# Kernel tuning notes

Hardware: AMD Instinct MI355X
Metric: run time of the kernel (lower is better)

Reference implementation:

```python
import math
import jax, jax.numpy as jnp
import numpy as np

H = 16  # num_heads
B, L, D = 1, 256, 1024


def setup_inputs() -> dict:
    key = jax.random.key(0)
    ks = jax.random.split(key, 12)
    s = 1.0 / math.sqrt(D)  # keep activations O(1)
    inp = {
        "mu": jax.random.normal(ks[0], (B, L, D), jnp.float32),
        "var": jax.random.uniform(ks[1], (B, L, D), jnp.float32) + 0.1,
    }
    names = ["q_mu", "q_var", "k_mu", "k_var", "v_mu", "v_var", "o_mu", "o_var"]
    for i, n in enumerate(names):
        inp["w" + n] = jax.random.normal(ks[2 + i], (D, D), jnp.float32) * s
        inp["b" + n] = jnp.zeros((D,), jnp.float32)
    return inp


def _split_heads(x):
    b, l, d = x.shape
    return x.reshape(b, l, H, d // H).transpose(0, 2, 1, 3)  # [B,H,L,Dh]


def _combine_heads(x):
    b, h, l, dh = x.shape
    return x.transpose(0, 2, 1, 3).reshape(b, l, h * dh)


def reference(mu, var, wq_mu, bq_mu, wq_var, bq_var, wk_mu, bk_mu, wk_var, bk_var,
              wv_mu, bv_mu, wv_var, bv_var, wo_mu, bo_mu, wo_var, bo_var):
    dk = mu.shape[-1] // H
    Qm = _split_heads(mu @ wq_mu + bq_mu)
    Qv = _split_heads(jax.nn.softplus(var @ wq_var + bq_var))
    Km = _split_heads(mu @ wk_mu + bk_mu)
    Kv = _split_heads(jax.nn.softplus(var @ wk_var + bk_var))
    Vm = _split_heads(mu @ wv_mu + bv_mu)
    Vv = _split_heads(jax.nn.softplus(var @ wv_var + bv_var))

    # per-element Gaussian KL, broadcast to [B,H,Lq,Lk,Dh] (as in the original)
    diff = (Qm[:, :, :, None, :] - Km[:, :, None, :, :]) ** 2
    ratio = Qv[:, :, :, None, :] / Kv[:, :, None, :, :]
    kl = diff / (2.0 * Kv[:, :, None, :, :]) + 0.5 * (ratio - jnp.log(ratio) - 1.0)
    scores = -kl.sum(-1) * (1.0 / math.sqrt(dk))  # [B,H,Lq,Lk]
    attn = jax.nn.softmax(scores, axis=-1)

    out_mu = jnp.einsum("bhqk,bhkd->bhqd", attn, Vm)
    out_var = jnp.einsum("bhqk,bhkd->bhqd", attn ** 2, Vv)

    O_mu = _combine_heads(out_mu)
    O_var = _combine_heads(out_var)
    mu_out = O_mu @ wo_mu + bo_mu
    var_out = jax.nn.softplus(O_var @ wo_var + bo_var)
    return mu_out, var_out
```

## Files before the change

kernel.cpp:

```cpp
#include <hip/hip_runtime.h>
#include <math.h>

typedef __bf16 bf16_t;
typedef bf16_t bf16x4 __attribute__((ext_vector_type(4)));
typedef bf16_t bf16x8 __attribute__((ext_vector_type(8)));
typedef float  f32x4  __attribute__((ext_vector_type(4)));

__device__ __forceinline__ float softplus_f(float x) {
    return (x > 20.f) ? x : log1pf(expf(x));
}

__device__ __forceinline__ float fast_rcp(float x) {
#if __has_builtin(__builtin_amdgcn_rcpf)
    return __builtin_amdgcn_rcpf(x);
#else
    return 1.0f / x;
#endif
}

struct PrepArgs { const float* src[8]; const float* mu; const float* var; };

__global__ __launch_bounds__(256) void prep_kernel(PrepArgs pa, bf16_t* __restrict__ wtbase,
                                                   bf16_t* __restrict__ dmu, bf16_t* __restrict__ dvar) {
    const int t = threadIdx.x;
    if (blockIdx.z == 8) {
        const int gid = (blockIdx.y * 16 + blockIdx.x) * 256 + t;
        const float* s; bf16_t* d; int off;
        if (gid < 32768) { s = pa.mu;  d = dmu;  off = gid * 8; }
        else             { s = pa.var; d = dvar; off = (gid - 32768) * 8; }
        float4 v0 = *(const float4*)(s + off);
        float4 v1 = *(const float4*)(s + off + 4);
        bf16x8 o;
        o[0] = (bf16_t)v0.x; o[1] = (bf16_t)v0.y; o[2] = (bf16_t)v0.z; o[3] = (bf16_t)v0.w;
        o[4] = (bf16_t)v1.x; o[5] = (bf16_t)v1.y; o[6] = (bf16_t)v1.z; o[7] = (bf16_t)v1.w;
        *(bf16x8*)(d + off) = o;
        return;
    }
    const int kt = blockIdx.x, nt = blockIdx.y, wm = blockIdx.z;
    const float* __restrict__ W = pa.src[wm];
    bf16_t* __restrict__ Wt = wtbase + (size_t)wm * 1048576;
    __shared__ bf16_t Ts[64][72];
    const int r0 = t >> 4, c4 = (t & 15) * 4;
#pragma unroll
    for (int rep = 0; rep < 4; ++rep) {
        const int r = r0 + rep * 16;
        const float4 v = *(const float4*)&W[(size_t)(kt * 64 + r) * 1024 + nt * 64 + c4];
        Ts[c4 + 0][r] = (bf16_t)v.x;
        Ts[c4 + 1][r] = (bf16_t)v.y;
        Ts[c4 + 2][r] = (bf16_t)v.z;
        Ts[c4 + 3][r] = (bf16_t)v.w;
    }
    __syncthreads();
#pragma unroll
    for (int rep = 0; rep < 2; ++rep) {
        const int chunk = t + rep * 256;
        const int n = chunk >> 3, kc = (chunk & 7) * 8;
        bf16x8 v = *(const bf16x8*)&Ts[n][kc];
        *(bf16x8*)&Wt[(size_t)(nt * 64 + n) * 1024 + kt * 64 + kc] = v;
    }
}

struct GemmArgs {
    const bf16_t* A[6];
    const bf16_t* Wt[6];
    const float*  bias[6];
    float*        dst[6];
    int           splus[6];
};

__global__ __launch_bounds__(256, 2) void gemm_splitk(GemmArgs args) {
    const int z = blockIdx.z;
    const bf16_t* __restrict__ A    = args.A[z];
    const bf16_t* __restrict__ Wt   = args.Wt[z];
    const float*  __restrict__ bias = args.bias[z];
    float*        __restrict__ dst  = args.dst[z];
    const int sp = args.splus[z];

    const int n_base = blockIdx.x * 64;
    const int m_base = blockIdx.y * 64;

    __shared__ __align__(16) unsigned char smem_raw[73728];
    bf16_t* stage = (bf16_t*)smem_raw;
    float*  Cr    = (float*)smem_raw;

    const int t = threadIdx.x;
    const int lane = t & 63;
    const int w = t >> 6;
    bf16_t* As = stage + w * 9216;
    bf16_t* Bs = As + 4608;

    const int r8 = lane >> 3, kb = lane & 7;
    const int fr = lane & 15, fq = lane >> 4, fk = fq * 8;

    const bf16_t* Ab = A  + (size_t)m_base * 1024 + w * 256 + kb * 8;
    const bf16_t* Bb = Wt + (size_t)n_base * 1024 + w * 256 + kb * 8;

    f32x4 acc[4][4] = {};

    bf16x8 pa[8], pb[8];
#pragma unroll
    for (int i = 0; i < 8; ++i) {
        pa[i] = *(const bf16x8*)(Ab + (size_t)(i * 8 + r8) * 1024);
        pb[i] = *(const bf16x8*)(Bb + (size_t)(i * 8 + r8) * 1024);
    }

#pragma unroll
    for (int s = 0; s < 4; ++s) {
#pragma unroll
        for (int i = 0; i < 8; ++i) {
            *(bf16x8*)&As[(i * 8 + r8) * 72 + kb * 8] = pa[i];
            *(bf16x8*)&Bs[(i * 8 + r8) * 72 + kb * 8] = pb[i];
        }
        if (s < 3) {
            const int off = (s + 1) * 64;
#pragma unroll
            for (int i = 0; i < 8; ++i) {
                pa[i] = *(const bf16x8*)(Ab + (size_t)(i * 8 + r8) * 1024 + off);
                pb[i] = *(const bf16x8*)(Bb + (size_t)(i * 8 + r8) * 1024 + off);
            }
        }
#pragma unroll
        for (int kh = 0; kh < 2; ++kh) {
            bf16x8 aF[4], bF[4];
#pragma unroll
            for (int i = 0; i < 4; ++i)
                aF[i] = *(const bf16x8*)&As[(i * 16 + fr) * 72 + kh * 32 + fk];
#pragma unroll
            for (int j = 0; j < 4; ++j)
                bF[j] = *(const bf16x8*)&Bs[(j * 16 + fr) * 72 + kh * 32 + fk];
#pragma unroll
            for (int i = 0; i < 4; ++i)
#pragma unroll
                for (int j = 0; j < 4; ++j)
                    acc[i][j] = __builtin_amdgcn_mfma_f32_16x16x32_bf16(aF[i], bF[j], acc[i][j], 0, 0, 0);
        }
    }

    __syncthreads();
    {
        float* Crw = Cr + w * 4352;
        const int orow = fq * 4;
#pragma unroll
        for (int i = 0; i < 4; ++i)
#pragma unroll
            for (int j = 0; j < 4; ++j)
#pragma unroll
                for (int rr = 0; rr < 4; ++rr)
                    Crw[(i * 16 + orow + rr) * 68 + j * 16 + fr] = acc[i][j][rr];
    }
    __syncthreads();

    const int cc = (t & 15) * 4;
    f32x4 bv4 = *(const f32x4*)&bias[n_base + cc];
#pragma unroll
    for (int i = 0; i < 4; ++i) {
        const int row = (t >> 4) + i * 16;
        f32x4 s0 = *(const f32x4*)&Cr[0 * 4352 + row * 68 + cc];
        f32x4 s1 = *(const f32x4*)&Cr[1 * 4352 + row * 68 + cc];
        f32x4 s2 = *(const f32x4*)&Cr[2 * 4352 + row * 68 + cc];
        f32x4 s3 = *(const f32x4*)&Cr[3 * 4352 + row * 68 + cc];
        f32x4 v = (s0 + s1) + (s2 + s3) + bv4;
        if (sp) {
            v[0] = softplus_f(v[0]); v[1] = softplus_f(v[1]);
            v[2] = softplus_f(v[2]); v[3] = softplus_f(v[3]);
        }
        *(f32x4*)&dst[(size_t)(m_base + row) * 1024 + n_base + cc] = v;
    }
}

__global__ __launch_bounds__(256) void feat_kernel(const float* __restrict__ Km,
                                                   const float* __restrict__ Kv,
                                                   bf16_t* __restrict__ Gbf,
                                                   float* __restrict__ cvec) {
    const int h = blockIdx.x, kb = blockIdx.y;
    const int t = threadIdx.x;
    const int kx = t & 63;
    const int dg = t >> 6;
    const int katt = kb * 64 + kx;
    const float* kvp = Kv + (size_t)katt * 1024 + h * 64 + dg * 16;
    const float* kmp = Km + (size_t)katt * 1024 + h * 64 + dg * 16;
    bf16_t* grow = Gbf + ((size_t)(h * 256 + katt)) * 128;
    float cp = 0.f;
#pragma unroll
    for (int c = 0; c < 4; ++c) {
        f32x4 kv = *(const f32x4*)(kvp + c * 4);
        f32x4 km = *(const f32x4*)(kmp + c * 4);
        bf16x4 o1, o2;
#pragma unroll
        for (int e = 0; e < 4; ++e) {
            const float r = 0.5f * fast_rcp(kv[e]);
            o1[e] = (bf16_t)r;
            o2[e] = (bf16_t)(-2.f * km[e] * r);
            cp += km[e] * km[e] * r + 0.5f * __logf(kv[e]);
        }
        *(bf16x4*)&grow[dg * 16 + c * 4]      = o1;
        *(bf16x4*)&grow[64 + dg * 16 + c * 4] = o2;
    }
    __shared__ float red[4][64];
    red[dg][kx] = cp;
    __syncthreads();
    if (dg == 0)
        cvec[h * 256 + katt] = red[0][kx] + red[1][kx] + red[2][kx] + red[3][kx];
}

#define OFF_VM   0
#define OFF_VV   36864
#define OFF_FS   73728
#define OFF_SC   82176
#define OFF_PHI  98816
#define OFF_PLO  107264
#define OFF_P2H  115712
#define OFF_P2L  124160
#define ATTN_SMEM 132608

__global__ __launch_bounds__(512) void attn_v7(const float* __restrict__ Qm,
                                               const float* __restrict__ Qv,
                                               const bf16_t* __restrict__ Gbf,
                                               const float* __restrict__ cvec,
                                               const float* __restrict__ Vm,
                                               const float* __restrict__ Vv,
                                               bf16_t* __restrict__ Omu,
                                               bf16_t* __restrict__ Ovar) {
    __shared__ __align__(16) unsigned char smem[ATTN_SMEM];
    bf16_t* Vsm = (bf16_t*)(smem + OFF_VM);
    bf16_t* Vsv = (bf16_t*)(smem + OFF_VV);
    float*  Fs  = (float*)(smem + OFF_FS);
    float*  Sc  = (float*)(smem + OFF_SC);
    bf16_t* Phi = (bf16_t*)(smem + OFF_PHI);
    bf16_t* Plo = (bf16_t*)(smem + OFF_PLO);
    bf16_t* P2h = (bf16_t*)(smem + OFF_P2H);
    bf16_t* P2l = (bf16_t*)(smem + OFF_P2L);

    const int qt = blockIdx.x, h = blockIdx.y;
    const int t = threadIdx.x, w = t >> 6, lane = t & 63;
    const int fr = lane & 15, fq = lane >> 4;
    const int n0 = w * 32;

    const bf16_t* gB = Gbf + ((size_t)(h * 256 + n0 + fr)) * 128 + fq * 8;

    bf16x8 bcur[4];
#pragma unroll
    for (int ks = 0; ks < 4; ++ks) bcur[ks] = *(const bf16x8*)(gB + ks * 32);

    if (t < 256) {
        const int r = t >> 4, c = t & 15;
        f32x4 qm = *(const f32x4*)(Qm + (size_t)(qt * 16 + r) * 1024 + h * 64 + c * 4);
        f32x4 qv = *(const f32x4*)(Qv + (size_t)(qt * 16 + r) * 1024 + h * 64 + c * 4);
        *(f32x4*)&Fs[r * 132 + c * 4]      = qm * qm + qv;
        *(f32x4*)&Fs[r * 132 + 64 + c * 4] = qm;
    }
    __syncthreads();

    bf16x8 ahi[4], alo[4];
#pragma unroll
    for (int ks = 0; ks < 4; ++ks) {
        f32x4 f0 = *(const f32x4*)&Fs[fr * 132 + ks * 32 + fq * 8];
        f32x4 f1 = *(const f32x4*)&Fs[fr * 132 + ks * 32 + fq * 8 + 4];
#pragma unroll
        for (int e = 0; e < 4; ++e) {
            bf16_t hb = (bf16_t)f0[e];
            ahi[ks][e] = hb; alo[ks][e] = (bf16_t)(f0[e] - (float)hb);
            bf16_t hb2 = (bf16_t)f1[e];
            ahi[ks][e + 4] = hb2; alo[ks][e + 4] = (bf16_t)(f1[e] - (float)hb2);
        }
    }

    const int tm = t & 255;
// ... 94 lines not shown
        *(bf16x4*)&P2h[row * 264 + lane * 4] = p2hi;
        *(bf16x4*)&P2l[row * 264 + lane * 4] = p2lo;
    }
    __syncthreads();

    const int tile = w & 3;
    const int isvar = w >> 2;
    const bf16_t* Pa = isvar ? P2h : Phi;
    const bf16_t* Pb = isvar ? P2l : Plo;
    const bf16_t* Vs = isvar ? Vsv : Vsm;
    f32x4 accp = {0.f, 0.f, 0.f, 0.f};
#pragma unroll
    for (int k0 = 0; k0 < 256; k0 += 32) {
        const int ka = k0 + fq * 8;
        bf16x8 a1 = *(const bf16x8*)&Pa[fr * 264 + ka];
        bf16x8 a2 = *(const bf16x8*)&Pb[fr * 264 + ka];
        bf16x8 bfr;
#pragma unroll
        for (int j = 0; j < 8; ++j)
            bfr[j] = Vs[(ka + j) * 72 + tile * 16 + fr];
        accp = __builtin_amdgcn_mfma_f32_16x16x32_bf16(a1, bfr, accp, 0, 0, 0);
        accp = __builtin_amdgcn_mfma_f32_16x16x32_bf16(a2, bfr, accp, 0, 0, 0);
    }

    bf16_t* Out = isvar ? Ovar : Omu;
#pragma unroll
    for (int reg = 0; reg < 4; ++reg) {
        const int qg = qt * 16 + fq * 4 + reg;
        const size_t ob = (size_t)qg * 1024 + h * 64 + tile * 16 + fr;
        Out[ob] = (bf16_t)accp[reg];
    }
}

extern "C" void kernel_launch(void* const* d_in, const int* in_sizes, int n_in,
                              void* d_out, int out_size, void* d_ws, size_t ws_size,
                              hipStream_t stream) {
    const float* mu  = (const float*)d_in[0];
    const float* var = (const float*)d_in[1];

    uint8_t* ws = (uint8_t*)d_ws;
    bf16_t* Abf_mu  = (bf16_t*)(ws);
    bf16_t* Abf_var = (bf16_t*)(ws + (512u << 10));
    bf16_t* WtB     = (bf16_t*)(ws + (1u << 20));
    float*  Proj    = (float*)(ws + (17u << 20));
    bf16_t* Obf_mu  = (bf16_t*)(ws + (23u << 20));
    bf16_t* Obf_var = (bf16_t*)(ws + (23u << 20) + (512u << 10));
    bf16_t* Gbf     = (bf16_t*)(ws + (24u << 20));
    float*  cvec    = (float*)(ws + (25u << 20));

    PrepArgs pa;
    for (int i = 0; i < 8; ++i) pa.src[i] = (const float*)d_in[2 + 2 * i];
    pa.mu = mu; pa.var = var;
    prep_kernel<<<dim3(16, 16, 9), 256, 0, stream>>>(pa, WtB, Abf_mu, Abf_var);

    GemmArgs g1;
    for (int z = 0; z < 6; ++z) {
        g1.A[z]    = (z & 1) ? Abf_var : Abf_mu;
        g1.Wt[z]   = WtB + (size_t)z * 1048576;
        g1.bias[z] = (const float*)d_in[3 + 2 * z];
        g1.dst[z]  = Proj + (size_t)z * 262144;
        g1.splus[z] = (z & 1);
    }
    gemm_splitk<<<dim3(16, 4, 6), 256, 0, stream>>>(g1);

    feat_kernel<<<dim3(16, 4), 256, 0, stream>>>(Proj + 2 * 262144, Proj + 3 * 262144, Gbf, cvec);

    attn_v7<<<dim3(16, 16), 512, 0, stream>>>(Proj,
                                              Proj + 262144,
                                              Gbf, cvec,
                                              Proj + 4 * 262144,
                                              Proj + 5 * 262144,
                                              Obf_mu, Obf_var);

    GemmArgs g3;
    for (int z = 0; z < 6; ++z) {
        g3.A[z]    = Obf_mu;
        g3.Wt[z]   = WtB + (size_t)6 * 1048576;
        g3.bias[z] = (const float*)d_in[15];
        g3.dst[z]  = (float*)d_out;
        g3.splus[z] = 0;
    }
    g3.A[1]    = Obf_var;
    g3.Wt[1]   = WtB + (size_t)7 * 1048576;
    g3.bias[1] = (const float*)d_in[17];
    g3.dst[1]  = (float*)d_out + 262144;
    g3.splus[1] = 1;
    gemm_splitk<<<dim3(16, 4, 2), 256, 0, stream>>>(g3);
}
```

Measured before the change: 150.4 us.

## Fuse whole pipeline into one cooperative persistent kernel with grid syncs

Replaces the chain of prep, projection GEMM, feature, attention and output GEMM launches with a single cooperative kernel of 256 blocks that runs each stage in turn, separated by grid-wide barriers. The projection GEMMs now read fp32 activations and convert them in-register, which removes the activation prep pass. The K projections are fused with the KL feature computation, and the GEMM K-split is widened to 8 waves. The aim is to cut launch overhead and intermediate passes, at the cost of grid-sync latency and fixed occupancy; the old multi-kernel path is kept as a fallback if the cooperative launch fails.

```diff
diff --git a/kernel.cpp b/kernel.cpp
--- a/kernel.cpp
+++ b/kernel.cpp
@@ -1,5 +1,8 @@
 #include <hip/hip_runtime.h>
+#include <hip/hip_cooperative_groups.h>
 #include <math.h>
+
+namespace cg = cooperative_groups;
 
 typedef __bf16 bf16_t;
 typedef bf16_t bf16x4 __attribute__((ext_vector_type(4)));
@@ -16,191 +19,6 @@
 #else
     return 1.0f / x;
 #endif
-}
-
-struct PrepArgs { const float* src[8]; const float* mu; const float* var; };
-
-__global__ __launch_bounds__(256) void prep_kernel(PrepArgs pa, bf16_t* __restrict__ wtbase,
-                                                   bf16_t* __restrict__ dmu, bf16_t* __restrict__ dvar) {
-    const int t = threadIdx.x;
-    if (blockIdx.z == 8) {
-        const int gid = (blockIdx.y * 16 + blockIdx.x) * 256 + t;
-        const float* s; bf16_t* d; int off;
-        if (gid < 32768) { s = pa.mu;  d = dmu;  off = gid * 8; }
-        else             { s = pa.var; d = dvar; off = (gid - 32768) * 8; }
-        float4 v0 = *(const float4*)(s + off);
-        float4 v1 = *(const float4*)(s + off + 4);
-        bf16x8 o;
-        o[0] = (bf16_t)v0.x; o[1] = (bf16_t)v0.y; o[2] = (bf16_t)v0.z; o[3] = (bf16_t)v0.w;
-        o[4] = (bf16_t)v1.x; o[5] = (bf16_t)v1.y; o[6] = (bf16_t)v1.z; o[7] = (bf16_t)v1.w;
-        *(bf16x8*)(d + off) = o;
-        return;
-    }
-    const int kt = blockIdx.x, nt = blockIdx.y, wm = blockIdx.z;
-    const float* __restrict__ W = pa.src[wm];
-    bf16_t* __restrict__ Wt = wtbase + (size_t)wm * 1048576;
-    __shared__ bf16_t Ts[64][72];
-    const int r0 = t >> 4, c4 = (t & 15) * 4;
-#pragma unroll
-    for (int rep = 0; rep < 4; ++rep) {
-        const int r = r0 + rep * 16;
-        const float4 v = *(const float4*)&W[(size_t)(kt * 64 + r) * 1024 + nt * 64 + c4];
-        Ts[c4 + 0][r] = (bf16_t)v.x;
-        Ts[c4 + 1][r] = (bf16_t)v.y;
-        Ts[c4 + 2][r] = (bf16_t)v.z;
-        Ts[c4 + 3][r] = (bf16_t)v.w;
-    }
-    __syncthreads();
-#pragma unroll
-    for (int rep = 0; rep < 2; ++rep) {
-        const int chunk = t + rep * 256;
-        const int n = chunk >> 3, kc = (chunk & 7) * 8;
-        bf16x8 v = *(const bf16x8*)&Ts[n][kc];
-        *(bf16x8*)&Wt[(size_t)(nt * 64 + n) * 1024 + kt * 64 + kc] = v;
-    }
-}
-
-struct GemmArgs {
-    const bf16_t* A[6];
-    const bf16_t* Wt[6];
-    const float*  bias[6];
-    float*        dst[6];
-    int           splus[6];
-};
-
-__global__ __launch_bounds__(256, 2) void gemm_splitk(GemmArgs args) {
-    const int z = blockIdx.z;
-    const bf16_t* __restrict__ A    = args.A[z];
-    const bf16_t* __restrict__ Wt   = args.Wt[z];
-    const float*  __restrict__ bias = args.bias[z];
-    float*        __restrict__ dst  = args.dst[z];
-    const int sp = args.splus[z];
-
-    const int n_base = blockIdx.x * 64;
-    const int m_base = blockIdx.y * 64;
-
-    __shared__ __align__(16) unsigned char smem_raw[73728];
-    bf16_t* stage = (bf16_t*)smem_raw;
-    float*  Cr    = (float*)smem_raw;
-
-    const int t = threadIdx.x;
-    const int lane = t & 63;
-    const int w = t >> 6;
-    bf16_t* As = stage + w * 9216;
-    bf16_t* Bs = As + 4608;
-
-    const int r8 = lane >> 3, kb = lane & 7;
-    const int fr = lane & 15, fq = lane >> 4, fk = fq * 8;
-
-    const bf16_t* Ab = A  + (size_t)m_base * 1024 + w * 256 + kb * 8;
-    const bf16_t* Bb = Wt + (size_t)n_base * 1024 + w * 256 + kb * 8;
-
-    f32x4 acc[4][4] = {};
-
-    bf16x8 pa[8], pb[8];
-#pragma unroll
-    for (int i = 0; i < 8; ++i) {
-        pa[i] = *(const bf16x8*)(Ab + (size_t)(i * 8 + r8) * 1024);
-        pb[i] = *(const bf16x8*)(Bb + (size_t)(i * 8 + r8) * 1024);
-    }
-
-#pragma unroll
-    for (int s = 0; s < 4; ++s) {
-#pragma unroll
-        for (int i = 0; i < 8; ++i) {
-            *(bf16x8*)&As[(i * 8 + r8) * 72 + kb * 8] = pa[i];
-            *(bf16x8*)&Bs[(i * 8 + r8) * 72 + kb * 8] = pb[i];
-        }
-        if (s < 3) {
-            const int off = (s + 1) * 64;
-#pragma unroll
-            for (int i = 0; i < 8; ++i) {
-                pa[i] = *(const bf16x8*)(Ab + (size_t)(i * 8 + r8) * 1024 + off);
-                pb[i] = *(const bf16x8*)(Bb + (size_t)(i * 8 + r8) * 1024 + off);
-            }
-        }
-#pragma unroll
-        for (int kh = 0; kh < 2; ++kh) {
-            bf16x8 aF[4], bF[4];
-#pragma unroll
-            for (int i = 0; i < 4; ++i)
-                aF[i] = *(const bf16x8*)&As[(i * 16 + fr) * 72 + kh * 32 + fk];
-#pragma unroll
-            for (int j = 0; j < 4; ++j)
-                bF[j] = *(const bf16x8*)&Bs[(j * 16 + fr) * 72 + kh * 32 + fk];
-#pragma unroll
-            for (int i = 0; i < 4; ++i)
-#pragma unroll
-                for (int j = 0; j < 4; ++j)
-                    acc[i][j] = __builtin_amdgcn_mfma_f32_16x16x32_bf16(aF[i], bF[j], acc[i][j], 0, 0, 0);
-        }
-    }
-
-    __syncthreads();
-    {
-        float* Crw = Cr + w * 4352;
-        const int orow = fq * 4;
-#pragma unroll
-        for (int i = 0; i < 4; ++i)
-#pragma unroll
-            for (int j = 0; j < 4; ++j)
-#pragma unroll
-                for (int rr = 0; rr < 4; ++rr)
-                    Crw[(i * 16 + orow + rr) * 68 + j * 16 + fr] = acc[i][j][rr];
-    }
-    __syncthreads();
-
-    const int cc = (t & 15) * 4;
-    f32x4 bv4 = *(const f32x4*)&bias[n_base + cc];
-#pragma unroll
-    for (int i = 0; i < 4; ++i) {
-        const int row = (t >> 4) + i * 16;
-        f32x4 s0 = *(const f32x4*)&Cr[0 * 4352 + row * 68 + cc];
-        f32x4 s1 = *(const f32x4*)&Cr[1 * 4352 + row * 68 + cc];
-        f32x4 s2 = *(const f32x4*)&Cr[2 * 4352 + row * 68 + cc];
-        f32x4 s3 = *(const f32x4*)&Cr[3 * 4352 + row * 68 + cc];
-        f32x4 v = (s0 + s1) + (s2 + s3) + bv4;
-        if (sp) {
-            v[0] = softplus_f(v[0]); v[1] = softplus_f(v[1]);
-            v[2] = softplus_f(v[2]); v[3] = softplus_f(v[3]);
-        }
-        *(f32x4*)&dst[(size_t)(m_base + row) * 1024 + n_base + cc] = v;
-    }
-}
-
-__global__ __launch_bounds__(256) void feat_kernel(const float* __restrict__ Km,
-                                                   const float* __restrict__ Kv,
-                                                   bf16_t* __restrict__ Gbf,
-                                                   float* __restrict__ cvec) {
-    const int h = blockIdx.x, kb = blockIdx.y;
-    const int t = threadIdx.x;
-    const int kx = t & 63;
-    const int dg = t >> 6;
-    const int katt = kb * 64 + kx;
-    const float* kvp = Kv + (size_t)katt * 1024 + h * 64 + dg * 16;
-    const float* kmp = Km + (size_t)katt * 1024 + h * 64 + dg * 16;
-    bf16_t* grow = Gbf + ((size_t)(h * 256 + katt)) * 128;
-    float cp = 0.f;
-#pragma unroll
-    for (int c = 0; c < 4; ++c) {
-        f32x4 kv = *(const f32x4*)(kvp + c * 4);
-        f32x4 km = *(const f32x4*)(kmp + c * 4);
-        bf16x4 o1, o2;
-#pragma unroll
-        for (int e = 0; e < 4; ++e) {
-            const float r = 0.5f * fast_rcp(kv[e]);
-            o1[e] = (bf16_t)r;
-            o2[e] = (bf16_t)(-2.f * km[e] * r);
-            cp += km[e] * km[e] * r + 0.5f * __logf(kv[e]);
-        }
-        *(bf16x4*)&grow[dg * 16 + c * 4]      = o1;
-        *(bf16x4*)&grow[64 + dg * 16 + c * 4] = o2;
-    }
-    __shared__ float red[4][64];
-    red[dg][kx] = cp;
-    __syncthreads();
-    if (dg == 0)
-        cvec[h * 256 + katt] = red[0][kx] + red[1][kx] + red[2][kx] + red[3][kx];
 }
 
 #define OFF_VM   0
@@ -213,15 +31,11 @@
 #define OFF_P2L  124160
 #define ATTN_SMEM 132608
 
-__global__ __launch_bounds__(512) void attn_v7(const float* __restrict__ Qm,
-                                               const float* __restrict__ Qv,
-                                               const bf16_t* __restrict__ Gbf,
-                                               const float* __restrict__ cvec,
-                                               const float* __restrict__ Vm,
-                                               const float* __restrict__ Vv,
-                                               bf16_t* __restrict__ Omu,
-                                               bf16_t* __restrict__ Ovar) {
-    __shared__ __align__(16) unsigned char smem[ATTN_SMEM];
+__device__ void attn_body(unsigned char* smem, const int t, const int qt, const int h,
+                          const float* __restrict__ Qm, const float* __restrict__ Qv,
+                          const bf16_t* __restrict__ Gbf, const float* __restrict__ cvec,
+                          const float* __restrict__ Vm, const float* __restrict__ Vv,
+                          bf16_t* __restrict__ Omu, bf16_t* __restrict__ Ovar) {
     bf16_t* Vsm = (bf16_t*)(smem + OFF_VM);
     bf16_t* Vsv = (bf16_t*)(smem + OFF_VV);
     float*  Fs  = (float*)(smem + OFF_FS);
@@ -231,8 +45,7 @@
     bf16_t* P2h = (bf16_t*)(smem + OFF_P2H);
     bf16_t* P2l = (bf16_t*)(smem + OFF_P2L);
 
-    const int qt = blockIdx.x, h = blockIdx.y;
-    const int t = threadIdx.x, w = t >> 6, lane = t & 63;
+    const int w = t >> 6, lane = t & 63;
     const int fr = lane & 15, fq = lane >> 4;
     const int n0 = w * 32;
 
@@ -393,13 +206,493 @@
     }
 }
 
+#define FUSED_SMEM 147456
+
+struct FusedArgs {
+    const float* mu; const float* var;
+    const float* W[8];
+    const float* Bias[8];
+    bf16_t* WtB;
+    float*  Proj;
+    bf16_t* Obm; bf16_t* Obv;
+    bf16_t* Gbf; float* cvec;
+    float* out_mu; float* out_var;
+};
+
+template<bool AF32>
+__device__ __forceinline__ void gemm_core(const void* Aptr, const bf16_t* __restrict__ Wt,
+                                          const int m_base, const int n_base,
+                                          unsigned char* smem, const int t, f32x4 out[2]) {
+    __syncthreads();
+    bf16_t* stage = (bf16_t*)smem;
+    float*  Cr    = (float*)smem;
+    const int lane = t & 63, w = t >> 6;
+    bf16_t* As = stage + w * 9216;
+    bf16_t* Bs = As + 4608;
+    const int r8 = lane >> 3, kb = lane & 7;
+    const int fr = lane & 15, fq = lane >> 4, fk = fq * 8;
+
+    const bf16_t* Bb = Wt + (size_t)n_base * 1024 + w * 128 + kb * 8;
+    const float*  Af = (const float*)Aptr  + (size_t)m_base * 1024 + w * 128 + kb * 8;
+    const bf16_t* Ab = (const bf16_t*)Aptr + (size_t)m_base * 1024 + w * 128 + kb * 8;
+
+    f32x4 acc[4][4] = {};
+    bf16x8 pb[8];
+    f32x4 paf0[8], paf1[8];
+    bf16x8 pa[8];
+#pragma unroll
+    for (int i = 0; i < 8; ++i) {
+        pb[i] = *(const bf16x8*)(Bb + (size_t)(i * 8 + r8) * 1024);
+        if constexpr (AF32) {
+            paf0[i] = *(const f32x4*)(Af + (size_t)(i * 8 + r8) * 1024);
+            paf1[i] = *(const f32x4*)(Af + (size_t)(i * 8 + r8) * 1024 + 4);
+        } else {
+            pa[i] = *(const bf16x8*)(Ab + (size_t)(i * 8 + r8) * 1024);
+        }
+    }
+
+#pragma unroll
+    for (int s = 0; s < 2; ++s) {
+#pragma unroll
+        for (int i = 0; i < 8; ++i) {
+            bf16x8 av;
+            if constexpr (AF32) {
+#pragma unroll
+                for (int e = 0; e < 4; ++e) {
+                    av[e]     = (bf16_t)paf0[i][e];
+                    av[e + 4] = (bf16_t)paf1[i][e];
+                }
+            } else {
+                av = pa[i];
+            }
+            *(bf16x8*)&As[(i * 8 + r8) * 72 + kb * 8] = av;
+            *(bf16x8*)&Bs[(i * 8 + r8) * 72 + kb * 8] = pb[i];
+        }
+        if (s == 0) {
+#pragma unroll
+            for (int i = 0; i < 8; ++i) {
+                pb[i] = *(const bf16x8*)(Bb + (size_t)(i * 8 + r8) * 1024 + 64);
+                if constexpr (AF32) {
+                    paf0[i] = *(const f32x4*)(Af + (size_t)(i * 8 + r8) * 1024 + 64);
+                    paf1[i] = *(const f32x4*)(Af + (size_t)(i * 8 + r8) * 1024 + 68);
+                } else {
+                    pa[i] = *(const bf16x8*)(Ab + (size_t)(i * 8 + r8) * 1024 + 64);
+                }
+            }
+        }
+#pragma unroll
+        for (int kh = 0; kh < 2; ++kh) {
+            bf16x8 aF[4], bF[4];
+#pragma unroll
+            for (int i = 0; i < 4; ++i)
+                aF[i] = *(const bf16x8*)&As[(i * 16 + fr) * 72 + kh * 32 + fk];
+#pragma unroll
+            for (int j = 0; j < 4; ++j)
+                bF[j] = *(const bf16x8*)&Bs[(j * 16 + fr) * 72 + kh * 32 + fk];
+#pragma unroll
+            for (int i = 0; i < 4; ++i)
+#pragma unroll
+                for (int j = 0; j < 4; ++j)
+                    acc[i][j] = __builtin_amdgcn_mfma_f32_16x16x32_bf16(aF[i], bF[j], acc[i][j], 0, 0, 0);
+        }
+    }
+
+    __syncthreads();
+    {
+        float* Crw = Cr + w * 4352;
+        const int orow = fq * 4;
+#pragma unroll
+        for (int i = 0; i < 4; ++i)
+#pragma unroll
+            for (int j = 0; j < 4; ++j)
+#pragma unroll
+                for (int rr = 0; rr < 4; ++rr)
+                    Crw[(i * 16 + orow + rr) * 68 + j * 16 + fr] = acc[i][j][rr];
+    }
+    __syncthreads();
+
+    const int cc = (t & 15) * 4;
+#pragma unroll
+    for (int i = 0; i < 2; ++i) {
+        const int row = (t >> 4) + i * 32;
+        f32x4 v = {0.f, 0.f, 0.f, 0.f};
+#pragma unroll
+        for (int sl = 0; sl < 8; ++sl)
+            v += *(const f32x4*)&Cr[sl * 4352 + row * 68 + cc];
+        out[i] = v;
+    }
+}
+
+__device__ __forceinline__ void run_simple(const FusedArgs& a, unsigned char* smem,
+                                           const int t, const int st) {
+    const int z4 = st >> 6, rem = st & 63;
+    const int nb = (rem >> 2) * 64, mb = (rem & 3) * 64;
+    const int wi = (z4 < 2) ? z4 : (z4 + 2);
+    const void* A = (z4 & 1) ? (const void*)a.var : (const void*)a.mu;
+    f32x4 o[2];
+    gemm_core<true>(A, a.WtB + (size_t)wi * 1048576, mb, nb, smem, t, o);
+    const int cc = (t & 15) * 4;
+    const f32x4 bv = *(const f32x4*)&a.Bias[wi][nb + cc];
+    float* dst = a.Proj + (size_t)z4 * 262144;
+    const int sp = z4 & 1;
+#pragma unroll
+    for (int i = 0; i < 2; ++i) {
+        const int row = (t >> 4) + i * 32;
+        f32x4 v = o[i] + bv;
+        if (sp) {
+            v[0] = softplus_f(v[0]); v[1] = softplus_f(v[1]);
+            v[2] = softplus_f(v[2]); v[3] = softplus_f(v[3]);
+        }
+        *(f32x4*)&dst[(size_t)(mb + row) * 1024 + nb + cc] = v;
+    }
+}
+
+__device__ __forceinline__ void run_fusedK(const FusedArgs& a, unsigned char* smem,
+                                           const int t, const int ft) {
+    const int nb = (ft >> 2) * 64, mb = (ft & 3) * 64;
+    const int h = ft >> 2;
+    f32x4 okm[2], okv[2];
+    gemm_core<true>(a.mu,  a.WtB + (size_t)2 * 1048576, mb, nb, smem, t, okm);
+    gemm_core<true>(a.var, a.WtB + (size_t)3 * 1048576, mb, nb, smem, t, okv);
+    const int cc = (t & 15) * 4;
+    const f32x4 bkm = *(const f32x4*)&a.Bias[2][nb + cc];
+    const f32x4 bkv = *(const f32x4*)&a.Bias[3][nb + cc];
+    float cp[2];
+#pragma unroll
+    for (int i = 0; i < 2; ++i) {
+        const int row = (t >> 4) + i * 32;
+        const int katt = mb + row;
+        const f32x4 km  = okm[i] + bkm;
+        const f32x4 kvr = okv[i] + bkv;
+        bf16x4 o1, o2;
+        float c = 0.f;
+#pragma unroll
+        for (int e = 0; e < 4; ++e) {
+            const float kv = softplus_f(kvr[e]);
+            const float r  = 0.5f * fast_rcp(kv);
+            o1[e] = (bf16_t)r;
+            o2[e] = (bf16_t)(-2.f * km[e] * r);
+            c += km[e] * km[e] * r + 0.5f * __logf(kv);
+        }
+        bf16_t* grow = a.Gbf + ((size_t)(h * 256 + katt)) * 128;
+        *(bf16x4*)&grow[cc]      = o1;
+        *(bf16x4*)&grow[64 + cc] = o2;
+        cp[i] = c;
+    }
+    __syncthreads();
+    float* red = (float*)smem;
+#pragma unroll
+    for (int i = 0; i < 2; ++i)
+        red[((t >> 4) + i * 32) * 16 + (t & 15)] = cp[i];
+    __syncthreads();
+    if (t < 64) {
+        float s = 0.f;
+#pragma unroll
+        for (int g = 0; g < 16; ++g) s += red[t * 16 + g];
+        a.cvec[h * 256 + mb + t] = s;
+    }
+}
+
+__global__ __launch_bounds__(512) void fused_all(FusedArgs a) {
+    __shared__ __align__(16) unsigned char smem[FUSED_SMEM];
+    cg::grid_group grid = cg::this_grid();
+    const int blk = blockIdx.x;
+    const int t = threadIdx.x;
+
+    {
+        bf16_t* Ts = (bf16_t*)smem + (t >> 8) * 4608;
+        const int lt = t & 255;
+        const int r0 = lt >> 4, c4 = (lt & 15) * 4;
+        for (int it = 0; it < 4; ++it) {
+            const int tt = blk * 8 + it * 2 + (t >> 8);
+            const int wm = tt >> 8, rem = tt & 255, kt = rem >> 4, nt = rem & 15;
+            const float* __restrict__ W = a.W[wm];
+            bf16_t* __restrict__ Wt = a.WtB + (size_t)wm * 1048576;
+#pragma unroll
+            for (int rep = 0; rep < 4; ++rep) {
+                const int r = r0 + rep * 16;
+                const float4 v = *(const float4*)&W[(size_t)(kt * 64 + r) * 1024 + nt * 64 + c4];
+                Ts[(c4 + 0) * 72 + r] = (bf16_t)v.x;
+                Ts[(c4 + 1) * 72 + r] = (bf16_t)v.y;
+                Ts[(c4 + 2) * 72 + r] = (bf16_t)v.z;
+                Ts[(c4 + 3) * 72 + r] = (bf16_t)v.w;
+            }
+            __syncthreads();
+#pragma unroll
+            for (int rep = 0; rep < 2; ++rep) {
+                const int chunk = lt + rep * 256;
+                const int n = chunk >> 3, kc = (chunk & 7) * 8;
+                bf16x8 v = *(const bf16x8*)&Ts[n * 72 + kc];
+                *(bf16x8*)&Wt[(size_t)(nt * 64 + n) * 1024 + kt * 64 + kc] = v;
+            }
+            __syncthreads();
+        }
+    }
+    __threadfence();
+    grid.sync();
+
+    if (blk < 192) {
+        run_simple(a, smem, t, blk);
+        if (blk < 64) run_simple(a, smem, t, 192 + blk);
+    } else {
+        run_fusedK(a, smem, t, blk - 192);
+    }
+    __threadfence();
+    grid.sync();
+
+    attn_body(smem, t, blk >> 4, blk & 15,
+              a.Proj, a.Proj + 262144, a.Gbf, a.cvec,
+              a.Proj + 2 * 262144, a.Proj + 3 * 262144, a.Obm, a.Obv);
+    __threadfence();
+    grid.sync();
+
+    if (blk < 128) {
+        const int z = blk >> 6, rem = blk & 63;
+        const int nb = (rem >> 2) * 64, mb = (rem & 3) * 64;
+        f32x4 o[2];
+        gemm_core<false>(z ? (const void*)a.Obv : (const void*)a.Obm,
+                         a.WtB + (size_t)(6 + z) * 1048576, mb, nb, smem, t, o);
+        const int cc = (t & 15) * 4;
+        const f32x4 bv = *(const f32x4*)&a.Bias[6 + z][nb + cc];
+        float* dst = z ? a.out_var : a.out_mu;
+#pragma unroll
+        for (int i = 0; i < 2; ++i) {
+            const int row = (t >> 4) + i * 32;
+            f32x4 v = o[i] + bv;
+            if (z) {
+                v[0] = softplus_f(v[0]); v[1] = softplus_f(v[1]);
+                v[2] = softplus_f(v[2]); v[3] = softplus_f(v[3]);
+            }
+            *(f32x4*)&dst[(size_t)(mb + row) * 1024 + nb + cc] = v;
+        }
+    }
+}
+
+struct PrepArgs { const float* src[8]; const float* mu; const float* var; };
+
+__global__ __launch_bounds__(256) void prep_kernel(PrepArgs pa, bf16_t* __restrict__ wtbase,
+                                                   bf16_t* __restrict__ dmu, bf16_t* __restrict__ dvar) {
+    const int t = threadIdx.x;
+    if (blockIdx.z == 8) {
+        const int gid = (blockIdx.y * 16 + blockIdx.x) * 256 + t;
+        const float* s; bf16_t* d; int off;
+        if (gid < 32768) { s = pa.mu;  d = dmu;  off = gid * 8; }
+        else             { s = pa.var; d = dvar; off = (gid - 32768) * 8; }
+        float4 v0 = *(const float4*)(s + off);
+        float4 v1 = *(const float4*)(s + off + 4);
+        bf16x8 o;
+        o[0] = (bf16_t)v0.x; o[1] = (bf16_t)v0.y; o[2] = (bf16_t)v0.z; o[3] = (bf16_t)v0.w;
+        o[4] = (bf16_t)v1.x; o[5] = (bf16_t)v1.y; o[6] = (bf16_t)v1.z; o[7] = (bf16_t)v1.w;
+        *(bf16x8*)(d + off) = o;
+        return;
+    }
+    const int kt = blockIdx.x, nt = blockIdx.y, wm = blockIdx.z;
+    const float* __restrict__ W = pa.src[wm];
+    bf16_t* __restrict__ Wt = wtbase + (size_t)wm * 1048576;
+    __shared__ bf16_t Ts[64][72];
+    const int r0 = t >> 4, c4 = (t & 15) * 4;
+#pragma unroll
+    for (int rep = 0; rep < 4; ++rep) {
+        const int r = r0 + rep * 16;
+        const float4 v = *(const float4*)&W[(size_t)(kt * 64 + r) * 1024 + nt * 64 + c4];
+        Ts[c4 + 0][r] = (bf16_t)v.x;
+        Ts[c4 + 1][r] = (bf16_t)v.y;
+        Ts[c4 + 2][r] = (bf16_t)v.z;
+        Ts[c4 + 3][r] = (bf16_t)v.w;
+    }
+    __syncthreads();
+#pragma unroll
+    for (int rep = 0; rep < 2; ++rep) {
+        const int chunk = t + rep * 256;
+        const int n = chunk >> 3, kc = (chunk & 7) * 8;
+        bf16x8 v = *(const bf16x8*)&Ts[n][kc];
+        *(bf16x8*)&Wt[(size_t)(nt * 64 + n) * 1024 + kt * 64 + kc] = v;
+    }
+}
+
+struct GemmArgs {
+    const bf16_t* A[6];
+    const bf16_t* Wt[6];
+    const float*  bias[6];
+    float*        dst[6];
+    int           splus[6];
+};
+
+__global__ __launch_bounds__(256, 2) void gemm_splitk(GemmArgs args) {
+    const int z = blockIdx.z;
+    const bf16_t* __restrict__ A    = args.A[z];
+    const bf16_t* __restrict__ Wt   = args.Wt[z];
+    const float*  __restrict__ bias = args.bias[z];
+    float*        __restrict__ dst  = args.dst[z];
+    const int sp = args.splus[z];
+
+    const int n_base = blockIdx.x * 64;
+    const int m_base = blockIdx.y * 64;
+
+    __shared__ __align__(16) unsigned char smem_raw[73728];
+    bf16_t* stage = (bf16_t*)smem_raw;
+    float*  Cr    = (float*)smem_raw;
+
+    const int t = threadIdx.x;
+    const int lane = t & 63;
+    const int w = t >> 6;
+    bf16_t* As = stage + w * 9216;
+    bf16_t* Bs = As + 4608;
+
+    const int r8 = lane >> 3, kb = lane & 7;
+    const int fr = lane & 15, fq = lane >> 4, fk = fq * 8;
+
+    const bf16_t* Ab = A  + (size_t)m_base * 1024 + w * 256 + kb * 8;
+    const bf16_t* Bb = Wt + (size_t)n_base * 1024 + w * 256 + kb * 8;
+
+    f32x4 acc[4][4] = {};
+
+    bf16x8 pa[8], pb[8];
+#pragma unroll
+    for (int i = 0; i < 8; ++i) {
+        pa[i] = *(const bf16x8*)(Ab + (size_t)(i * 8 + r8) * 1024);
+        pb[i] = *(const bf16x8*)(Bb + (size_t)(i * 8 + r8) * 1024);
+    }
+
+#pragma unroll
+    for (int s = 0; s < 4; ++s) {
+#pragma unroll
+        for (int i = 0; i < 8; ++i) {
+            *(bf16x8*)&As[(i * 8 + r8) * 72 + kb * 8] = pa[i];
+            *(bf16x8*)&Bs[(i * 8 + r8) * 72 + kb * 8] = pb[i];
+        }
+        if (s < 3) {
+            const int off = (s + 1) * 64;
+#pragma unroll
+            for (int i = 0; i < 8; ++i) {
+                pa[i] = *(const bf16x8*)(Ab + (size_t)(i * 8 + r8) * 1024 + off);
+                pb[i] = *(const bf16x8*)(Bb + (size_t)(i * 8 + r8) * 1024 + off);
+            }
+        }
+#pragma unroll
+        for (int kh = 0; kh < 2; ++kh) {
+            bf16x8 aF[4], bF[4];
+#pragma unroll
+            for (int i = 0; i < 4; ++i)
+                aF[i] = *(const bf16x8*)&As[(i * 16 + fr) * 72 + kh * 32 + fk];
+#pragma unroll
+            for (int j = 0; j < 4; ++j)
+                bF[j] = *(const bf16x8*)&Bs[(j * 16 + fr) * 72 + kh * 32 + fk];
+#pragma unroll
+            for (int i = 0; i < 4; ++i)
+#pragma unroll
+                for (int j = 0; j < 4; ++j)
+                    acc[i][j] = __builtin_amdgcn_mfma_f32_16x16x32_bf16(aF[i], bF[j], acc[i][j], 0, 0, 0);
+        }
+    }
+
+    __syncthreads();
+    {
+        float* Crw = Cr + w * 4352;
+        const int orow = fq * 4;
+#pragma unroll
+        for (int i = 0; i < 4; ++i)
+#pragma unroll
+            for (int j = 0; j < 4; ++j)
+#pragma unroll
+                for (int rr = 0; rr < 4; ++rr)
+                    Crw[(i * 16 + orow + rr) * 68 + j * 16 + fr] = acc[i][j][rr];
+    }
+    __syncthreads();
+
+    const int cc = (t & 15) * 4;
+    f32x4 bv4 = *(const f32x4*)&bias[n_base + cc];
+#pragma unroll
+    for (int i = 0; i < 4; ++i) {
+        const int row = (t >> 4) + i * 16;
+        f32x4 s0 = *(const f32x4*)&Cr[0 * 4352 + row * 68 + cc];
+        f32x4 s1 = *(const f32x4*)&Cr[1 * 4352 + row * 68 + cc];
+        f32x4 s2 = *(const f32x4*)&Cr[2 * 4352 + row * 68 + cc];
+        f32x4 s3 = *(const f32x4*)&Cr[3 * 4352 + row * 68 + cc];
+        f32x4 v = (s0 + s1) + (s2 + s3) + bv4;
+        if (sp) {
+            v[0] = softplus_f(v[0]); v[1] = softplus_f(v[1]);
+            v[2] = softplus_f(v[2]); v[3] = softplus_f(v[3]);
+        }
+        *(f32x4*)&dst[(size_t)(m_base + row) * 1024 + n_base + cc] = v;
+    }
+}
+
+__global__ __launch_bounds__(256) void feat_kernel(const float* __restrict__ Km,
+                                                   const float* __restrict__ Kv,
+                                                   bf16_t* __restrict__ Gbf,
+                                                   float* __restrict__ cvec) {
+    const int h = blockIdx.x, kb = blockIdx.y;
+    const int t = threadIdx.x;
+    const int kx = t & 63;
+    const int dg = t >> 6;
+    const int katt = kb * 64 + kx;
+    const float* kvp = Kv + (size_t)katt * 1024 + h * 64 + dg * 16;
+    const float* kmp = Km + (size_t)katt * 1024 + h * 64 + dg * 16;
+    bf16_t* grow = Gbf + ((size_t)(h * 256 + katt)) * 128;
+    float cp = 0.f;
+#pragma unroll
+    for (int c = 0; c < 4; ++c) {
+        f32x4 kv = *(const f32x4*)(kvp + c * 4);
+        f32x4 km = *(const f32x4*)(kmp + c * 4);
+        bf16x4 o1, o2;
+#pragma unroll
+        for (int e = 0; e < 4; ++e) {
+            const float r = 0.5f * fast_rcp(kv[e]);
+            o1[e] = (bf16_t)r;
+            o2[e] = (bf16_t)(-2.f * km[e] * r);
+            cp += km[e] * km[e] * r + 0.5f * __logf(kv[e]);
+        }
+        *(bf16x4*)&grow[dg * 16 + c * 4]      = o1;
+        *(bf16x4*)&grow[64 + dg * 16 + c * 4] = o2;
+    }
+    __shared__ float red[4][64];
+    red[dg][kx] = cp;
+    __syncthreads();
+    if (dg == 0)
+        cvec[h * 256 + katt] = red[0][kx] + red[1][kx] + red[2][kx] + red[3][kx];
+}
+
+__global__ __launch_bounds__(512) void attn_v7(const float* __restrict__ Qm,
+                                               const float* __restrict__ Qv,
+                                               const bf16_t* __restrict__ Gbf,
+                                               const float* __restrict__ cvec,
+                                               const float* __restrict__ Vm,
+                                               const float* __restrict__ Vv,
+                                               bf16_t* __restrict__ Omu,
+                                               bf16_t* __restrict__ Ovar) {
+    __shared__ __align__(16) unsigned char smem[ATTN_SMEM];
+    attn_body(smem, threadIdx.x, blockIdx.x, blockIdx.y, Qm, Qv, Gbf, cvec, Vm, Vv, Omu, Ovar);
+}
+
 extern "C" void kernel_launch(void* const* d_in, const int* in_sizes, int n_in,
                               void* d_out, int out_size, void* d_ws, size_t ws_size,
                               hipStream_t stream) {
     const float* mu  = (const float*)d_in[0];
     const float* var = (const float*)d_in[1];
-
     uint8_t* ws = (uint8_t*)d_ws;
+
+    FusedArgs fa;
+    fa.mu = mu; fa.var = var;
+    for (int i = 0; i < 8; ++i) {
+        fa.W[i]    = (const float*)d_in[2 + 2 * i];
+        fa.Bias[i] = (const float*)d_in[3 + 2 * i];
+    }
+    fa.WtB  = (bf16_t*)(ws);
+    fa.Proj = (float*)(ws + (16u << 20));
+    fa.Obm  = (bf16_t*)(ws + (20u << 20));
+    fa.Obv  = (bf16_t*)(ws + (20u << 20) + (512u << 10));
+    fa.Gbf  = (bf16_t*)(ws + (21u << 20));
+    fa.cvec = (float*)(ws + (22u << 20));
+    fa.out_mu  = (float*)d_out;
+    fa.out_var = (float*)d_out + 262144;
+
+    void* kp[] = { &fa };
+    hipError_t err = hipLaunchCooperativeKernel((void*)fused_all, dim3(256), dim3(512),
+                                                kp, 0, stream);
+    if (err == hipSuccess) return;
+    (void)hipGetLastError();
+
     bf16_t* Abf_mu  = (bf16_t*)(ws);
     bf16_t* Abf_var = (bf16_t*)(ws + (512u << 10));
     bf16_t* WtB     = (bf16_t*)(ws + (1u << 20));
@@ -426,11 +719,8 @@
 
     feat_kernel<<<dim3(16, 4), 256, 0, stream>>>(Proj + 2 * 262144, Proj + 3 * 262144, Gbf, cvec);
 
-    attn_v7<<<dim3(16, 16), 512, 0, stream>>>(Proj,
-                                              Proj + 262144,
-                                              Gbf, cvec,
-                                              Proj + 4 * 262144,
-                                              Proj + 5 * 262144,
+    attn_v7<<<dim3(16, 16), 512, 0, stream>>>(Proj, Proj + 262144, Gbf, cvec,
+                                              Proj + 4 * 262144, Proj + 5 * 262144,
                                               Obf_mu, Obf_var);
 
     GemmArgs g3;
```

New measurement: 396.1 us. +163.4%, slower.

## Fuse input bf16 cast into projection GEMM and K-feature prep into K-projection

Applied to the files above, without the earlier changes.

The projection GEMM now reads the fp32 mu/var directly and converts them to bf16 while staging into LDS, so the separate cast pass in the prep kernel is gone. The K-mean and K-variance projections are computed together in one block, which then writes the Gbf features and the cvec constants directly, removing feat_kernel and the fp32 Km/Kv round-trip through global memory. This saves one launch and some traffic, but the fused K blocks do two GEMMs each, creating a slower tail within a grid of 320 blocks. The fp32 A loads also double the A-side load bytes and register use.

```diff
diff --git a/kernel.cpp b/kernel.cpp
--- a/kernel.cpp
+++ b/kernel.cpp
@@ -18,24 +18,10 @@
 #endif
 }
 
-struct PrepArgs { const float* src[8]; const float* mu; const float* var; };
-
-__global__ __launch_bounds__(256) void prep_kernel(PrepArgs pa, bf16_t* __restrict__ wtbase,
-                                                   bf16_t* __restrict__ dmu, bf16_t* __restrict__ dvar) {
+struct PrepArgs { const float* src[8]; };
+
+__global__ __launch_bounds__(256) void prep_kernel(PrepArgs pa, bf16_t* __restrict__ wtbase) {
     const int t = threadIdx.x;
-    if (blockIdx.z == 8) {
-        const int gid = (blockIdx.y * 16 + blockIdx.x) * 256 + t;
-        const float* s; bf16_t* d; int off;
-        if (gid < 32768) { s = pa.mu;  d = dmu;  off = gid * 8; }
-        else             { s = pa.var; d = dvar; off = (gid - 32768) * 8; }
-        float4 v0 = *(const float4*)(s + off);
-        float4 v1 = *(const float4*)(s + off + 4);
-        bf16x8 o;
-        o[0] = (bf16_t)v0.x; o[1] = (bf16_t)v0.y; o[2] = (bf16_t)v0.z; o[3] = (bf16_t)v0.w;
-        o[4] = (bf16_t)v1.x; o[5] = (bf16_t)v1.y; o[6] = (bf16_t)v1.z; o[7] = (bf16_t)v1.w;
-        *(bf16x8*)(d + off) = o;
-        return;
-    }
     const int kt = blockIdx.x, nt = blockIdx.y, wm = blockIdx.z;
     const float* __restrict__ W = pa.src[wm];
     bf16_t* __restrict__ Wt = wtbase + (size_t)wm * 1048576;
@@ -60,63 +46,65 @@
     }
 }
 
-struct GemmArgs {
-    const bf16_t* A[6];
-    const bf16_t* Wt[6];
-    const float*  bias[6];
-    float*        dst[6];
-    int           splus[6];
-};
-
-__global__ __launch_bounds__(256, 2) void gemm_splitk(GemmArgs args) {
-    const int z = blockIdx.z;
-    const bf16_t* __restrict__ A    = args.A[z];
-    const bf16_t* __restrict__ Wt   = args.Wt[z];
-    const float*  __restrict__ bias = args.bias[z];
-    float*        __restrict__ dst  = args.dst[z];
-    const int sp = args.splus[z];
-
-    const int n_base = blockIdx.x * 64;
-    const int m_base = blockIdx.y * 64;
-
-    __shared__ __align__(16) unsigned char smem_raw[73728];
-    bf16_t* stage = (bf16_t*)smem_raw;
-    float*  Cr    = (float*)smem_raw;
-
-    const int t = threadIdx.x;
-    const int lane = t & 63;
-    const int w = t >> 6;
+template<bool AF32>
+__device__ __forceinline__ void gemm4_core(const void* Aptr, const bf16_t* __restrict__ Wt,
+                                           const int m_base, const int n_base,
+                                           unsigned char* smem, const int t, f32x4 out[4]) {
+    __syncthreads();
+    bf16_t* stage = (bf16_t*)smem;
+    float*  Cr    = (float*)smem;
+    const int lane = t & 63, w = t >> 6;
     bf16_t* As = stage + w * 9216;
     bf16_t* Bs = As + 4608;
-
     const int r8 = lane >> 3, kb = lane & 7;
     const int fr = lane & 15, fq = lane >> 4, fk = fq * 8;
 
-    const bf16_t* Ab = A  + (size_t)m_base * 1024 + w * 256 + kb * 8;
     const bf16_t* Bb = Wt + (size_t)n_base * 1024 + w * 256 + kb * 8;
+    const float*  Af = (const float*)Aptr  + (size_t)m_base * 1024 + w * 256 + kb * 8;
+    const bf16_t* Ab = (const bf16_t*)Aptr + (size_t)m_base * 1024 + w * 256 + kb * 8;
 
     f32x4 acc[4][4] = {};
-
     bf16x8 pa[8], pb[8];
+    f32x4 paf0[8], paf1[8];
 #pragma unroll
     for (int i = 0; i < 8; ++i) {
-        pa[i] = *(const bf16x8*)(Ab + (size_t)(i * 8 + r8) * 1024);
         pb[i] = *(const bf16x8*)(Bb + (size_t)(i * 8 + r8) * 1024);
+        if constexpr (AF32) {
+            paf0[i] = *(const f32x4*)(Af + (size_t)(i * 8 + r8) * 1024);
+            paf1[i] = *(const f32x4*)(Af + (size_t)(i * 8 + r8) * 1024 + 4);
+        } else {
+            pa[i] = *(const bf16x8*)(Ab + (size_t)(i * 8 + r8) * 1024);
+        }
     }
 
 #pragma unroll
     for (int s = 0; s < 4; ++s) {
 #pragma unroll
         for (int i = 0; i < 8; ++i) {
-            *(bf16x8*)&As[(i * 8 + r8) * 72 + kb * 8] = pa[i];
+            bf16x8 av;
+            if constexpr (AF32) {
+#pragma unroll
+                for (int e = 0; e < 4; ++e) {
+                    av[e]     = (bf16_t)paf0[i][e];
+                    av[e + 4] = (bf16_t)paf1[i][e];
+                }
+            } else {
+                av = pa[i];
+            }
+            *(bf16x8*)&As[(i * 8 + r8) * 72 + kb * 8] = av;
             *(bf16x8*)&Bs[(i * 8 + r8) * 72 + kb * 8] = pb[i];
         }
         if (s < 3) {
             const int off = (s + 1) * 64;
 #pragma unroll
             for (int i = 0; i < 8; ++i) {
-                pa[i] = *(const bf16x8*)(Ab + (size_t)(i * 8 + r8) * 1024 + off);
                 pb[i] = *(const bf16x8*)(Bb + (size_t)(i * 8 + r8) * 1024 + off);
+                if constexpr (AF32) {
+                    paf0[i] = *(const f32x4*)(Af + (size_t)(i * 8 + r8) * 1024 + off);
+                    paf1[i] = *(const f32x4*)(Af + (size_t)(i * 8 + r8) * 1024 + off + 4);
+                } else {
+                    pa[i] = *(const bf16x8*)(Ab + (size_t)(i * 8 + r8) * 1024 + off);
+                }
             }
         }
 #pragma unroll
@@ -151,7 +139,6 @@
     __syncthreads();
 
     const int cc = (t & 15) * 4;
-    f32x4 bv4 = *(const f32x4*)&bias[n_base + cc];
 #pragma unroll
     for (int i = 0; i < 4; ++i) {
         const int row = (t >> 4) + i * 16;
@@ -159,48 +146,77 @@
         f32x4 s1 = *(const f32x4*)&Cr[1 * 4352 + row * 68 + cc];
         f32x4 s2 = *(const f32x4*)&Cr[2 * 4352 + row * 68 + cc];
         f32x4 s3 = *(const f32x4*)&Cr[3 * 4352 + row * 68 + cc];
-        f32x4 v = (s0 + s1) + (s2 + s3) + bv4;
-        if (sp) {
-            v[0] = softplus_f(v[0]); v[1] = softplus_f(v[1]);
-            v[2] = softplus_f(v[2]); v[3] = softplus_f(v[3]);
-        }
-        *(f32x4*)&dst[(size_t)(m_base + row) * 1024 + n_base + cc] = v;
-    }
-}
-
-__global__ __launch_bounds__(256) void feat_kernel(const float* __restrict__ Km,
-                                                   const float* __restrict__ Kv,
-                                                   bf16_t* __restrict__ Gbf,
-                                                   float* __restrict__ cvec) {
-    const int h = blockIdx.x, kb = blockIdx.y;
+        out[i] = (s0 + s1) + (s2 + s3);
+    }
+}
+
+struct ProjArgs {
+    const float* mu; const float* var;
+    const bf16_t* WtB;
+    const float* bias[6];
+    float* Proj;
+    bf16_t* Gbf; float* cvec;
+};
+
+__global__ __launch_bounds__(256, 2) void proj_kernel(ProjArgs a) {
+    __shared__ __align__(16) unsigned char smem[73728];
+    const int z = blockIdx.z;
+    const int nb = blockIdx.x * 64, mb = blockIdx.y * 64;
     const int t = threadIdx.x;
-    const int kx = t & 63;
-    const int dg = t >> 6;
-    const int katt = kb * 64 + kx;
-    const float* kvp = Kv + (size_t)katt * 1024 + h * 64 + dg * 16;
-    const float* kmp = Km + (size_t)katt * 1024 + h * 64 + dg * 16;
-    bf16_t* grow = Gbf + ((size_t)(h * 256 + katt)) * 128;
-    float cp = 0.f;
-#pragma unroll
-    for (int c = 0; c < 4; ++c) {
-        f32x4 kv = *(const f32x4*)(kvp + c * 4);
-        f32x4 km = *(const f32x4*)(kmp + c * 4);
-        bf16x4 o1, o2;
-#pragma unroll
-        for (int e = 0; e < 4; ++e) {
-            const float r = 0.5f * fast_rcp(kv[e]);
-            o1[e] = (bf16_t)r;
-            o2[e] = (bf16_t)(-2.f * km[e] * r);
-            cp += km[e] * km[e] * r + 0.5f * __logf(kv[e]);
-        }
-        *(bf16x4*)&grow[dg * 16 + c * 4]      = o1;
-        *(bf16x4*)&grow[64 + dg * 16 + c * 4] = o2;
-    }
-    __shared__ float red[4][64];
-    red[dg][kx] = cp;
-    __syncthreads();
-    if (dg == 0)
-        cvec[h * 256 + katt] = red[0][kx] + red[1][kx] + red[2][kx] + red[3][kx];
+    const int cc = (t & 15) * 4;
+
+    if (z != 2) {
+        const int wi   = (z < 2) ? z : (z + 1);
+        const int slot = (z < 2) ? z : (z - 1);
+        const int sp   = (z == 1) || (z == 4);
+        const void* A  = (z == 1 || z == 4) ? (const void*)a.var : (const void*)a.mu;
+        f32x4 o[4];
+        gemm4_core<true>(A, a.WtB + (size_t)wi * 1048576, mb, nb, smem, t, o);
+        const f32x4 bv = *(const f32x4*)&a.bias[wi][nb + cc];
+        float* dst = a.Proj + (size_t)slot * 262144;
+#pragma unroll
+        for (int i = 0; i < 4; ++i) {
+            const int row = (t >> 4) + i * 16;
+            f32x4 v = o[i] + bv;
+            if (sp) {
+                v[0] = softplus_f(v[0]); v[1] = softplus_f(v[1]);
+                v[2] = softplus_f(v[2]); v[3] = softplus_f(v[3]);
+            }
+            *(f32x4*)&dst[(size_t)(mb + row) * 1024 + nb + cc] = v;
+        }
+    } else {
+        const int h = blockIdx.x;
+        f32x4 okm[4], okv[4];
+        gemm4_core<true>(a.mu,  a.WtB + (size_t)2 * 1048576, mb, nb, smem, t, okm);
+        gemm4_core<true>(a.var, a.WtB + (size_t)3 * 1048576, mb, nb, smem, t, okv);
+        const f32x4 bkm = *(const f32x4*)&a.bias[2][nb + cc];
+        const f32x4 bkv = *(const f32x4*)&a.bias[3][nb + cc];
+#pragma unroll
+        for (int i = 0; i < 4; ++i) {
+            const int row = (t >> 4) + i * 16;
+            const int katt = mb + row;
+            const f32x4 km  = okm[i] + bkm;
+            const f32x4 kvr = okv[i] + bkv;
+            bf16x4 o1, o2;
+            float c = 0.f;
+#pragma unroll
+            for (int e = 0; e < 4; ++e) {
+                const float kv = softplus_f(kvr[e]);
+                const float r  = 0.5f * fast_rcp(kv);
+                o1[e] = (bf16_t)r;
+                o2[e] = (bf16_t)(-2.f * km[e] * r);
+                c += km[e] * km[e] * r + 0.5f * __logf(kv);
+            }
+            bf16_t* grow = a.Gbf + ((size_t)(h * 256 + katt)) * 128;
+            *(bf16x4*)&grow[cc]      = o1;
+            *(bf16x4*)&grow[64 + cc] = o2;
+#pragma unroll
+            for (int off = 8; off > 0; off >>= 1)
+                c += __shfl_xor(c, off, 16);
+            if ((t & 15) == 0)
+                a.cvec[h * 256 + katt] = c;
+        }
+    }
 }
 
 #define OFF_VM   0
@@ -393,58 +409,78 @@
     }
 }
 
+struct OutArgs {
+    const bf16_t* A[2];
+    const bf16_t* Wt[2];
+    const float*  bias[2];
+    float*        dst[2];
+    int           splus[2];
+};
+
+__global__ __launch_bounds__(256, 2) void out_gemm(OutArgs args) {
+    const int z = blockIdx.z;
+    const bf16_t* __restrict__ A    = args.A[z];
+    const bf16_t* __restrict__ Wt   = args.Wt[z];
+    const float*  __restrict__ bias = args.bias[z];
+    float*        __restrict__ dst  = args.dst[z];
+    const int sp = args.splus[z];
+
+    const int n_base = blockIdx.x * 64;
+    const int m_base = blockIdx.y * 64;
+
+    __shared__ __align__(16) unsigned char smem[73728];
+    const int t = threadIdx.x;
+    f32x4 o[4];
+    gemm4_core<false>(A, Wt, m_base, n_base, smem, t, o);
+
+    const int cc = (t & 15) * 4;
+    const f32x4 bv = *(const f32x4*)&bias[n_base + cc];
+#pragma unroll
+    for (int i = 0; i < 4; ++i) {
+        const int row = (t >> 4) + i * 16;
+        f32x4 v = o[i] + bv;
+        if (sp) {
+            v[0] = softplus_f(v[0]); v[1] = softplus_f(v[1]);
+            v[2] = softplus_f(v[2]); v[3] = softplus_f(v[3]);
+        }
+        *(f32x4*)&dst[(size_t)(m_base + row) * 1024 + n_base + cc] = v;
+    }
+}
+
 extern "C" void kernel_launch(void* const* d_in, const int* in_sizes, int n_in,
                               void* d_out, int out_size, void* d_ws, size_t ws_size,
                               hipStream_t stream) {
     const float* mu  = (const float*)d_in[0];
     const float* var = (const float*)d_in[1];
-
     uint8_t* ws = (uint8_t*)d_ws;
-    bf16_t* Abf_mu  = (bf16_t*)(ws);
-    bf16_t* Abf_var = (bf16_t*)(ws + (512u << 10));
-    bf16_t* WtB     = (bf16_t*)(ws + (1u << 20));
-    float*  Proj    = (float*)(ws + (17u << 20));
-    bf16_t* Obf_mu  = (bf16_t*)(ws + (23u << 20));
-    bf16_t* Obf_var = (bf16_t*)(ws + (23u << 20) + (512u << 10));
-    bf16_t* Gbf     = (bf16_t*)(ws + (24u << 20));
-    float*  cvec    = (float*)(ws + (25u << 20));
+
+    bf16_t* WtB  = (bf16_t*)(ws);
+    float*  Proj = (float*)(ws + (16u << 20));
+    bf16_t* Obm  = (bf16_t*)(ws + (20u << 20));
+    bf16_t* Obv  = (bf16_t*)(ws + (20u << 20) + (512u << 10));
+    bf16_t* Gbf  = (bf16_t*)(ws + (21u << 20));
+    float*  cvec = (float*)(ws + (22u << 20));
 
     PrepArgs pa;
     for (int i = 0; i < 8; ++i) pa.src[i] = (const float*)d_in[2 + 2 * i];
-    pa.mu = mu; pa.var = var;
-    prep_kernel<<<dim3(16, 16, 9), 256, 0, stream>>>(pa, WtB, Abf_mu, Abf_var);
-
-    GemmArgs g1;
-    for (int z = 0; z < 6; ++z) {
-        g1.A[z]    = (z & 1) ? Abf_var : Abf_mu;
-        g1.Wt[z]   = WtB + (size_t)z * 1048576;
-        g1.bias[z] = (const float*)d_in[3 + 2 * z];
-        g1.dst[z]  = Proj + (size_t)z * 262144;
-        g1.splus[z] = (z & 1);
-    }
-    gemm_splitk<<<dim3(16, 4, 6), 256, 0, stream>>>(g1);
-
-    feat_kernel<<<dim3(16, 4), 256, 0, stream>>>(Proj + 2 * 262144, Proj + 3 * 262144, Gbf, cvec);
-
-    attn_v7<<<dim3(16, 16), 512, 0, stream>>>(Proj,
-                                              Proj + 262144,
-                                              Gbf, cvec,
-                                              Proj + 4 * 262144,
-                                              Proj + 5 * 262144,
-                                              Obf_mu, Obf_var);
-
-    GemmArgs g3;
-    for (int z = 0; z < 6; ++z) {
-        g3.A[z]    = Obf_mu;
-        g3.Wt[z]   = WtB + (size_t)6 * 1048576;
-        g3.bias[z] = (const float*)d_in[15];
-        g3.dst[z]  = (float*)d_out;
-        g3.splus[z] = 0;
-    }
-    g3.A[1]    = Obf_var;
-    g3.Wt[1]   = WtB + (size_t)7 * 1048576;
+    prep_kernel<<<dim3(16, 16, 8), 256, 0, stream>>>(pa, WtB);
+
+    ProjArgs pr;
+    pr.mu = mu; pr.var = var; pr.WtB = WtB;
+    for (int i = 0; i < 6; ++i) pr.bias[i] = (const float*)d_in[3 + 2 * i];
+    pr.Proj = Proj; pr.Gbf = Gbf; pr.cvec = cvec;
+    proj_kernel<<<dim3(16, 4, 5), 256, 0, stream>>>(pr);
+
+    attn_v7<<<dim3(16, 16), 512, 0, stream>>>(Proj, Proj + 262144, Gbf, cvec,
+                                              Proj + 2 * 262144, Proj + 3 * 262144,
+                                              Obm, Obv);
+
+    OutArgs g3;
+    g3.A[0] = Obm;  g3.Wt[0] = WtB + (size_t)6 * 1048576;
+    g3.bias[0] = (const float*)d_in[15];
+    g3.dst[0] = (float*)d_out;             g3.splus[0] = 0;
+    g3.A[1] = Obv;  g3.Wt[1] = WtB + (size_t)7 * 1048576;
     g3.bias[1] = (const float*)d_in[17];
-    g3.dst[1]  = (float*)d_out + 262144;
-    g3.splus[1] = 1;
-    gemm_splitk<<<dim3(16, 4, 2), 256, 0, stream>>>(g3);
-}
+    g3.dst[1] = (float*)d_out + 262144;    g3.splus[1] = 1;
+    out_gemm<<<dim3(16, 4, 2), 256, 0, stream>>>(g3);
+}
```

After: 150.8 us. No clear change (+0.3%).
